# Performance work log

Measured on AMD Instinct MI355X. Metric: run time of the kernel, lower is better.

## Reference

```python
import jax, jax.numpy as jnp
import numpy as np

H, W, V = 32, 64, 13
B, C_IN = 8, 256
RADIUS = 6371.0 * 1000.0
NUM_LAT = H + 2
_j = np.arange(1, NUM_LAT - 1, dtype=np.float64)
_LATS = (90.0 - _j * 180.0 / (NUM_LAT - 1)) * np.pi / 180.0  # [32] radians
PIXEL_X = jnp.asarray(2.0 * np.pi * RADIUS * np.cos(_LATS) / W, dtype=jnp.float32).reshape(1, 1, H, 1)
PIXEL_Y = np.float32(np.pi * RADIUS / (H + 1))
_DZ = np.array([50, 50, 50, 50, 50, 75, 100, 100, 100, 125, 112, 75, 75], dtype=np.float32)
PIXEL_Z = jnp.asarray(_DZ).reshape(1, V, 1, 1)
PRESSURE = jnp.asarray([50, 100, 150, 200, 250, 300, 400, 500, 600, 700, 850, 925, 1000], dtype=jnp.float32).reshape(1, V, 1, 1)
M_Z = jnp.asarray(np.tril(np.ones((V, V), dtype=np.float32)) * _DZ[None, :])  # lower-tri integration matrix
LAT_GRID = jnp.asarray(_LATS, dtype=jnp.float32).reshape(1, 1, H, 1)

OMEGA, L_V, R_GAS, C_P, R_D = 7.29e-5, 2.5e6, 8.314, 1005.0, 287.0
DIFF_RATIO, DT, K_H, K_V = 0.05, 300.0, 15.0, 0.1
SIGMA, EMIS, PTHRESH = 5.67e-8, 0.7, 0.8
sg = jax.lax.stop_gradient


def d_x(f):  # periodic 4th-order diff along W, kernel [1,-8,0,8,-1]/12
    g = (jnp.roll(f, 2, 3) - 8.0 * jnp.roll(f, 1, 3) + 8.0 * jnp.roll(f, -1, 3) - jnp.roll(f, -2, 3)) / 12.0
    return g / PIXEL_X


def d_y(f):  # replicate-block padding along H, kernel [-1,8,0,-8,1]/12
    p = jnp.concatenate([f[:, :, :2], f, f[:, :, -2:]], axis=2)
    g = (-p[:, :, :-4] + 8.0 * p[:, :, 1:-3] - 8.0 * p[:, :, 3:-1] + p[:, :, 4:]) / 12.0
    return g / PIXEL_Y


def d_z(f):  # replicate-block padding along level dim (axis 1)
    p = jnp.concatenate([f[:, :2], f, f[:, -2:]], axis=1)
    g = (-p[:, :-4] + 8.0 * p[:, 1:-3] - 8.0 * p[:, 3:-1] + p[:, 4:]) / 12.0
    return g / PIXEL_Z


def integral_z(f):
    return jnp.einsum('ij,bjhw->bihw', M_Z, f)


def conv3x3(x, w, b):
    y = jax.lax.conv_general_dilated(x, w, (1, 1), ((1, 1), (1, 1)), dimension_numbers=('NCHW', 'OIHW', 'NCHW'))
    return y + b[None, :, None, None]


def batchnorm(x, g, b, eps=1e-5):  # training-mode BN (batch statistics)
    m = x.mean(axis=(0, 2, 3), keepdims=True)
    v = x.var(axis=(0, 2, 3), keepdims=True)
    return (x - m) / jnp.sqrt(v + eps) * g.reshape(1, -1, 1, 1) + b.reshape(1, -1, 1, 1)


def scale_tensor(t, a, b):
    mn, mx = sg(t.min()), sg(t.max())
    return (t - mn) / (mx - mn) * (b - a) + a


def scale_diff(d, x):
    mn, me, mx = sg(x.min()), sg(x.mean()), sg(x.max())
    return scale_tensor(d, (mn - me) * DIFF_RATIO, (mx - me) * DIFF_RATIO)


def avoid_inf(t, thr=1.0):
    t = jnp.where(jnp.abs(t) == 0.0, jnp.full_like(t, 0.1), t)
    return jnp.where(jnp.abs(t) < thr, jnp.sign(t) * thr, t)


def mixing(f):
    return K_H * (d_x(d_x(f)) + d_y(d_y(f))) + K_V * d_z(d_z(f))


def rad_cool(t):
    ta = t + 273.15
    return -(EMIS * SIGMA * ta ** 4) / (C_P * PRESSURE * 100.0 / (R_D * ta))


def saturation(t, z_z):
    rho = -1.0 / avoid_inf(z_z)
    p = rho * R_GAS * t
    tc = t - 273.15
    e_s = 6.112 * jnp.exp(scale_tensor(17.67 * tc / avoid_inf(tc + 243.5), -3.47, 3.01)) * 100.0
    return jnp.maximum(0.622 * e_s / avoid_inf(p - 0.378 * e_s), 1e-6)


def precip(q, q_s):
    rh = q / avoid_inf(q_s)
    rate = (rh > PTHRESH).astype(q.dtype) * (q - PTHRESH * q_s) / DT
    return rate, rate * L_V / C_P


def uv_dt(u, v, w, u_x, v_y, z_x, z_y):
    # u_x, v_y are held fixed across RK stages (stateful self.u_x/self.v_y in the original)
    f_cor = 2.0 * OMEGA * jnp.sin(LAT_GRID)
    u_t = -u * u_x - v * d_y(u) - w * d_z(u) + f_cor * v - z_x + mixing(u)
    v_t = -u * d_x(v) - v * v_y - w * d_z(v) - f_cor * u - z_y + mixing(v)
    return u_t, v_t


def t_dt(u, v, w, t, q, q_s, z_z):
    Q = -L_V * z_z * w
    _, lh = precip(q, q_s)
    return (Q - z_z * w) / C_P - u * d_x(t) - v * d_y(t) - w * d_z(t) + mixing(t) + rad_cool(t) + lh


def pde_forward(x, w_norm, b_norm, w_innorm, b_innorm, coef, gz, bz, gq, bq, gu, bu, gv, bv, gt, bt, gblk, bblk):
    h = conv3x3(x, w_norm, b_norm)  # [B, 65, H, W]
    z, q, u, v, t = jnp.split(h, 5, axis=1)
    z = batchnorm(z, gz, bz); q = batchnorm(q, gq, bq)
    u = batchnorm(u, gu, bu); v = batchnorm(v, gv, bv); t = batchnorm(t, gt, bt)
    z_x, z_y, z_z = d_x(z), d_y(z), d_z(z)
    u_x, v_y = d_x(u), d_y(v)
    w_vel = -integral_z(u_x + v_y)  # continuity: dw/dz = -(u_x + v_y)
    # --- RK4 momentum evolution ---
    k1u, k1v = uv_dt(u, v, w_vel, u_x, v_y, z_x, z_y)
    k2u, k2v = uv_dt(u + 0.5 * DT * k1u, v + 0.5 * DT * k1v, w_vel, u_x, v_y, z_x, z_y)
    k3u, k3v = uv_dt(u + 0.5 * DT * k2u, v + 0.5 * DT * k2v, w_vel, u_x, v_y, z_x, z_y)
    k4u, k4v = uv_dt(u + DT * k3u, v + DT * k3v, w_vel, u_x, v_y, z_x, z_y)
    u_new = u + sg(scale_diff((k1u + 2 * k2u + 2 * k3u + k4u) / 6.0 * DT, u))
    v_new = v + sg(scale_diff((k1v + 2 * k2v + 2 * k3v + k4v) / 6.0 * DT, v))
    # --- RK4 temperature evolution (q_s fixed from initial t) ---
    q_s = saturation(t, z_z)
    k1t = t_dt(u, v, w_vel, t, q, q_s, z_z)
    k2t = t_dt(u, v, w_vel, t + 0.5 * DT * k1t, q, q_s, z_z)
    k3t = t_dt(u, v, w_vel, t + 0.5 * DT * k2t, q, q_s, z_z)
    k4t = t_dt(u, v, w_vel, t + DT * k3t, q, q_s, z_z)
    t_new = t + sg(scale_diff((k1t + 2 * k2t + 2 * k3t + k4t) / 6.0 * DT, t))
    # geopotential tendency uses stateful self.t_t (last computed stage = k4t)
    z_t = integral_z(-R_GAS / PRESSURE * k4t)
    z_new = z + sg(scale_diff(z_t * DT, z))
    # moisture evolution
    pr, _ = precip(q, q_s)
    q_t = -u * d_x(q) - v * d_y(q) - w_vel * d_z(q) + mixing(q) - pr
    q_new = q + sg(scale_diff(q_t * DT, q))
    phys = jnp.concatenate([z_new, q_new, u_new, v_new, t_new], axis=1)
    out = coef * phys + (1.0 - coef) * h
    out = conv3x3(out, w_innorm, b_innorm)
    return batchnorm(out, gblk, bblk) + x


def setup_inputs() -> dict:
    key = jax.random.key(0)
    k0, k1, k2 = jax.random.split(key, 3)
    VD = V * 5
    ones13 = jnp.ones((V,), jnp.float32)
    zeros13 = jnp.zeros((V,), jnp.float32)
    return {
        'x': jax.random.normal(k0, (B, C_IN, H, W), jnp.float32),
        'w_norm': jax.random.normal(k1, (VD, C_IN, 3, 3), jnp.float32) * 0.02,
        'b_norm': jnp.zeros((VD,), jnp.float32),
        'w_innorm': jax.random.normal(k2, (C_IN, VD, 3, 3), jnp.float32) * 0.02,
        'b_innorm': jnp.zeros((C_IN,), jnp.float32),
        'coef': 0.5 * jnp.ones((1, VD, H, W), jnp.float32),
        'gz': 0.1 * ones13, 'bz': zeros13,
        'gq': 0.1 * ones13, 'bq': zeros13,
        'gu': 0.1 * ones13, 'bu': zeros13,
        'gv': 0.1 * ones13, 'bv': zeros13,
        'gt': 0.1 * ones13, 'bt': zeros13,
        'gblk': jnp.ones((C_IN,), jnp.float32),
        'bblk': jnp.zeros((C_IN,), jnp.float32),
    }


def reference(x, w_norm, b_norm, w_innorm, b_innorm, coef, gz, bz, gq, bq, gu, bu, gv, bv, gt, bt, gblk, bblk):
    return pde_forward(x, w_norm, b_norm, w_innorm, b_innorm, coef, gz, bz, gq, bq, gu, bu, gv, bv, gt, bt, gblk, bblk)
```

## Files before the change

### kernel.cpp

```cpp
#include <hip/hip_runtime.h>
#include <math.h>

#define DEVFN static __device__ __forceinline__

static constexpr int BB = 8, VV = 13, HH = 32, WW = 64;
static constexpr int NPLANE = HH * WW;
static constexpr int NF = BB * VV * NPLANE;
static constexpr int NHB = BB * 65 * NPLANE;

static constexpr float DT = 300.0f;
static constexpr float KHc = 15.0f, KVc = 0.1f;
static constexpr float OMEGAc = 7.29e-5f;
static constexpr float L_Vc = 2.5e6f;
static constexpr float R_GASc = 8.314f;
static constexpr float C_Pc = 1005.0f;
static constexpr float PTHc = 0.8f;
static constexpr float PYc  = (float)(3.14159265358979323846 * 6371000.0 / 33.0);
static constexpr float PXCc = (float)(2.0 * 3.14159265358979323846 * 6371000.0 / 64.0);
static constexpr double RCCd = 0.7 * 5.67e-8 * 287.0 / (1005.0 * 100.0);
static constexpr float FBIG = 3.402823466e38f;

__constant__ float cDZ[13]  = {50,50,50,50,50,75,100,100,100,125,112,75,75};
__constant__ float cZI[13] = {
  (float)(1.0/600.0), (float)(1.0/600.0), (float)(1.0/600.0), (float)(1.0/600.0), (float)(1.0/600.0),
  (float)(1.0/900.0), (float)(1.0/1200.0), (float)(1.0/1200.0), (float)(1.0/1200.0),
  (float)(1.0/1500.0), (float)(1.0/1344.0), (float)(1.0/900.0), (float)(1.0/900.0)};
__constant__ float cRC[13] = {
  (float)(-RCCd/50.0), (float)(-RCCd/100.0), (float)(-RCCd/150.0), (float)(-RCCd/200.0),
  (float)(-RCCd/250.0), (float)(-RCCd/300.0), (float)(-RCCd/400.0), (float)(-RCCd/500.0),
  (float)(-RCCd/600.0), (float)(-RCCd/700.0), (float)(-RCCd/850.0), (float)(-RCCd/925.0),
  (float)(-RCCd/1000.0)};
__constant__ float cZW[13] = {
  (float)(50.0*(-8.314/50.0)), (float)(50.0*(-8.314/100.0)), (float)(50.0*(-8.314/150.0)),
  (float)(50.0*(-8.314/200.0)), (float)(50.0*(-8.314/250.0)), (float)(75.0*(-8.314/300.0)),
  (float)(100.0*(-8.314/400.0)), (float)(100.0*(-8.314/500.0)), (float)(100.0*(-8.314/600.0)),
  (float)(125.0*(-8.314/700.0)), (float)(112.0*(-8.314/850.0)), (float)(75.0*(-8.314/925.0)),
  (float)(75.0*(-8.314/1000.0))};

typedef short bf16x8 __attribute__((ext_vector_type(8)));
typedef float f32x4 __attribute__((ext_vector_type(4)));

DEVFN int pmh(int r){ return r < 0 ? r + 2 : (r > HH - 1 ? r - 2 : r); }
DEVFN int pmv(int r){ return r < 0 ? r + 2 : (r > VV - 1 ? r - 2 : r); }
DEVFN float latOf(int h){ return (90.0f - (float)(h + 1) * (180.0f / 33.0f)) * 0.017453292519943295f; }
DEVFN float avoid_inf(float t){
  if (t == 0.0f) t = 0.1f;
  if (fabsf(t) < 1.0f) t = copysignf(1.0f, t);
  return t;
}
DEVFN unsigned short f2bf(float f){
  unsigned u = __float_as_uint(f);
  unsigned r = (u + 0x7fffu + ((u >> 16) & 1u)) >> 16;
  return (unsigned short)r;
}

DEVFN float d_xf(const float* __restrict__ F, int rb, int w, float invpx){
  return (F[rb + ((w + 62) & 63)] - 8.f * F[rb + ((w + 63) & 63)]
        + 8.f * F[rb + ((w + 1) & 63)] - F[rb + ((w + 2) & 63)]) * (1.f / 12.f) * invpx;
}
DEVFN float d_yf(const float* __restrict__ F, int bvbase, int h, int w){
  return (-F[bvbase + pmh(h - 2) * 64 + w] + 8.f * F[bvbase + pmh(h - 1) * 64 + w]
          - 8.f * F[bvbase + pmh(h + 1) * 64 + w] + F[bvbase + pmh(h + 2) * 64 + w]) * (1.f / 12.f) * (1.f / PYc);
}
DEVFN float d_zf(const float* __restrict__ F, int bbase, int v, int hw){
  return (-F[bbase + pmv(v - 2) * 2048 + hw] + 8.f * F[bbase + pmv(v - 1) * 2048 + hw]
          - 8.f * F[bbase + pmv(v + 1) * 2048 + hw] + F[bbase + pmv(v + 2) * 2048 + hw]) * cZI[v];
}
DEVFN float dxxf(const float* __restrict__ F, int rb, int w, float invpx){
  float s = F[rb + ((w + 60) & 63)] - 16.f * F[rb + ((w + 61) & 63)] + 64.f * F[rb + ((w + 62) & 63)]
          + 16.f * F[rb + ((w + 63) & 63)] - 130.f * F[rb + w] + 16.f * F[rb + ((w + 1) & 63)]
          + 64.f * F[rb + ((w + 2) & 63)] - 16.f * F[rb + ((w + 3) & 63)] + F[rb + ((w + 4) & 63)];
  return s * (1.f / 144.f) * invpx * invpx;
}
DEVFN float dyyf(const float* __restrict__ F, int bvbase, int h, int w){
  float g0 = d_yf(F, bvbase, pmh(h - 2), w);
  float g1 = d_yf(F, bvbase, pmh(h - 1), w);
  float g2 = d_yf(F, bvbase, pmh(h + 1), w);
  float g3 = d_yf(F, bvbase, pmh(h + 2), w);
  return (-g0 + 8.f * g1 - 8.f * g2 + g3) * (1.f / 12.f) * (1.f / PYc);
}
DEVFN float dzzf(const float* __restrict__ F, int bbase, int v, int hw){
  float g0 = d_zf(F, bbase, pmv(v - 2), hw);
  float g1 = d_zf(F, bbase, pmv(v - 1), hw);
  float g2 = d_zf(F, bbase, pmv(v + 1), hw);
  float g3 = d_zf(F, bbase, pmv(v + 2), hw);
  return (-g0 + 8.f * g1 - 8.f * g2 + g3) * cZI[v];
}

DEVFN float waveRedSum(float v){ for (int o = 32; o; o >>= 1) v += __shfl_down(v, o, 64); return v; }
DEVFN float waveRedMin(float v){ for (int o = 32; o; o >>= 1) v = fminf(v, __shfl_down(v, o, 64)); return v; }
DEVFN float waveRedMax(float v){ for (int o = 32; o; o >>= 1) v = fmaxf(v, __shfl_down(v, o, 64)); return v; }

template<int OP, int NWV>
static __device__ float blockRedN(float v){
  __shared__ float s[NWV];
  v = OP == 0 ? waveRedSum(v) : OP == 1 ? waveRedMin(v) : waveRedMax(v);
  int lane = threadIdx.x & 63, wid = threadIdx.x >> 6;
  __syncthreads();
  if (lane == 0) s[wid] = v;
  __syncthreads();
  float r = s[0];
  #pragma unroll
  for (int k = 1; k < NWV; ++k)
    r = OP == 0 ? r + s[k] : OP == 1 ? fminf(r, s[k]) : fmaxf(r, s[k]);
  return r;
}

struct GB { const float* g[5]; const float* b[5]; };

__global__ void __launch_bounds__(256) pre_k(const float* __restrict__ x,
    const float* __restrict__ w1, const float* __restrict__ w2,
    unsigned short* __restrict__ XT, unsigned short* __restrict__ wp1,
    unsigned short* __restrict__ wp2)
{
  int blk = blockIdx.x, t = threadIdx.x;
  if (blk < 1024){
    __shared__ float tile[16 * 68];
    int zz = blk >> 8, rem = blk & 255;
    int b = rem >> 5, h = rem & 31;
    for (int p = zz * 4; p < zz * 4 + 4; ++p){
      int cbase = p * 16;
      __syncthreads();
      {
        int cl = t >> 4, w4 = (t & 15) * 4;
        float4 v = *(const float4*)(x + (((size_t)(b * 256 + cbase + cl) * 32 + h) * 64 + w4));
        tile[cl * 68 + w4 + 0] = v.x; tile[cl * 68 + w4 + 1] = v.y;
        tile[cl * 68 + w4 + 2] = v.z; tile[cl * 68 + w4 + 3] = v.w;
      }
      __syncthreads();
      {
        int w = t >> 2, c4 = (t & 3) * 4;
        ushort4 o;
        o.x = f2bf(tile[(c4 + 0) * 68 + w]);
        o.y = f2bf(tile[(c4 + 1) * 68 + w]);
        o.z = f2bf(tile[(c4 + 2) * 68 + w]);
        o.w = f2bf(tile[(c4 + 3) * 68 + w]);
        *(ushort4*)(XT + (((size_t)(b * 32 + h) * 64 + w) * 256 + cbase + c4)) = o;
      }
    }
  } else {
    const int T1 = 9 * 80 * 256;
    const int T2 = 9 * 256 * 96;
    int idx = (blk - 1024) * 256 + t;
    if (idx < T1){
      int dir = idx / (80 * 256);
      int r = idx - dir * (80 * 256);
      int co = r / 256, ci = r - co * 256;
      float v = (co < 65) ? w1[((size_t)(co * 256 + ci)) * 9 + dir] : 0.f;
      wp1[idx] = f2bf(v);
    } else if (idx < T1 + T2){
      int j = idx - T1;
      int dir = j / (256 * 96);
      int r = j - dir * (256 * 96);
      int co = r / 96, ci = r - co * 96;
      float v = (ci < 65) ? w2[((size_t)(co * 65 + ci)) * 9 + dir] : 0.f;
      wp2[j] = f2bf(v);
    }
  }
}

template<int CIT, int CIL, int CO, int COp, int NW, int MF, int SWZ>
__global__ void __launch_bounds__(NW * 64) conv_mfma_k(
    const unsigned short* __restrict__ XT, const unsigned short* __restrict__ Wp,
    const float* __restrict__ bias, float* __restrict__ out, float* __restrict__ bnp)
{
  __shared__ __align__(16) unsigned short Xl[3 * 34 * CIL];
  const int C8 = CIL / 8;
  int tid = threadIdx.x;
  int bx = blockIdx.x, b = blockIdx.y;
  int h = bx >> 1, p0 = (bx & 1) << 5;
  int bh = b * 64 + bx;
  int wid = tid >> 6, lane = tid & 63;
  int l15 = lane & 15, q = lane >> 4;

  f32x4 acc[MF][2];
  #pragma unroll
  for (int mf = 0; mf < MF; ++mf)
    #pragma unroll
    for (int nf = 0; nf < 2; ++nf){ f32x4 z = {0.f, 0.f, 0.f, 0.f}; acc[mf][nf] = z; }

  for (int cp = 0; cp < CIT / CIL; ++cp){
    if (cp) __syncthreads();
    for (int idx = tid; idx < 3 * 34 * C8; idx += NW * 64){
      int r = idx / (34 * C8);
      int rest = idx - r * (34 * C8);
      int j = rest / C8;
      int c8 = rest - j * C8;
      int hh = h + r - 1;
      int gw = p0 - 1 + j;
      uint4 val = make_uint4(0, 0, 0, 0);
      if (hh >= 0 && hh < 32 && gw >= 0 && gw < 64)
        val = *(const uint4*)(XT + (((size_t)(b * 32 + hh) * 64 + gw) * CIT + cp * CIL + c8 * 8));
      int dst = (r * 34 + j) * CIL + ((c8 * 8) ^ ((j & SWZ) << 3));
      *(uint4*)(Xl + dst) = val;
    }
    __syncthreads();

    for (int dir = 0; dir < 9; ++dir){
      int dy = dir / 3, dx = dir - dy * 3;
      #pragma unroll
      for (int kc = 0; kc < CIL / 32; ++kc){
        int kb = kc * 32 + q * 8;
        bf16x8 a[MF];
        #pragma unroll
        for (int mf = 0; mf < MF; ++mf){
          int co = wid * (MF * 16) + mf * 16 + l15;
          a[mf] = *(const bf16x8*)(Wp + ((size_t)(dir * COp + co) * CIT + cp * CIL + kb));
        }
        #pragma unroll
        for (int nf = 0; nf < 2; ++nf){
          int j = nf * 16 + l15 + dx;
          bf16x8 bfrag = *(const bf16x8*)(Xl + ((dy * 34 + j) * CIL + (kb ^ ((j & SWZ) << 3))));
          #pragma unroll
          for (int mf = 0; mf < MF; ++mf)
            acc[mf][nf] = __builtin_amdgcn_mfma_f32_16x16x32_bf16(a[mf], bfrag, acc[mf][nf], 0, 0, 0);
        }
      }
    }
  }
  #pragma unroll
  for (int mf = 0; mf < MF; ++mf){
    #pragma unroll
    for (int r = 0; r < 4; ++r){
      int co = wid * (MF * 16) + mf * 16 + q * 4 + r;
      if (CO != COp && co >= CO) continue;
      float bv = bias[co];
      float sv = 0.f, sq = 0.f;
      #pragma unroll
      for (int nf = 0; nf < 2; ++nf){
        int pix = nf * 16 + l15;
        float val = acc[mf][nf][r] + bv;
        out[(size_t)(b * CO + co) * 2048 + h * 64 + p0 + pix] = val;
        sv += val; sq += val * val;
      }
      #pragma unroll
      for (int off = 8; off; off >>= 1){
        sv += __shfl_xor(sv, off, 16);
        sq += __shfl_xor(sq, off, 16);
      }
      if (l15 == 0){
        bnp[((size_t)co * 512 + bh) * 2]     = sv;
        bnp[((size_t)co * 512 + bh) * 2 + 1] = sq;
      }
    }
  }
}

__global__ void __launch_bounds__(256) prep_k(const float* __restrict__ hb,
  const float* __restrict__ bnp1, GB gb,
  float* __restrict__ Fz, float* __restrict__ Fq, float* __restrict__ Fu,
  float* __restrict__ Fvf, float* __restrict__ Ft,
  float* __restrict__ zx, float* __restrict__ zy, float* __restrict__ zz,
  float* __restrict__ ux, float* __restrict__ vy, float* __restrict__ wv,
  float* __restrict__ partS)
{
  __shared__ float As[65], Bs[65];
  int blk = blockIdx.x, t = threadIdx.x;
  {
    int wvid = t >> 6, lane = t & 63;
    for (int ch = wvid; ch < 65; ch += 4){
      const float4* pp = (const float4*)(bnp1 + (size_t)ch * 1024) + lane * 4;
      float s = 0.f, sq = 0.f;
      #pragma unroll
      for (int k = 0; k < 4; ++k){ float4 v = pp[k]; s += v.x + v.z; sq += v.y + v.w; }
      s = waveRedSum(s); sq = waveRedSum(sq);
      if (!lane){
        float m = s * (1.f / 16384.f);
        float var = sq * (1.f / 16384.f) - m * m;
        float rstd = rsqrtf(var + 1e-5f);
        int f = ch / 13, k = ch - f * 13;
        float g = gb.g[f][k], bbv = gb.b[f][k];
        As[ch] = g * rstd; Bs[ch] = bbv - m * g * rstd;
      }
    }
  }
  __syncthreads();

  int part = blk >> 6;
  int col = ((blk & 63) << 8) | t;
  int b = col >> 11, p = col & 2047, h = p >> 6, w = p & 63;
  int hbase = b * 65 * NPLANE;
  auto hn = [&](int ch, int hh, int ww)->float {
    return hb[hbase + ch * 2048 + hh * 64 + ww] * As[ch] + Bs[ch];
  };
  int fb = (b * 13) * 2048 + p;
  float lat = latOf(h);
  float invpx = 1.0f / (PXCc * cosf(lat));
  int wm2 = (w + 62) & 63, wm1 = (w + 63) & 63, wpl1 = (w + 1) & 63, wpl2 = (w + 2) & 63;
  int hm2 = pmh(h - 2), hm1 = pmh(h - 1), hp1 = pmh(h + 1), hp2 = pmh(h + 2);
  float fmn = FBIG, fmx = -FBIG, fsm = 0.f, smn = FBIG, smx = -FBIG;
  if (part < 5){
    int ch0 = part * 13;
    float c[13];
    #pragma unroll
    for (int v = 0; v < 13; ++v) c[v] = hn(ch0 + v, h, w);
    float* Fdst = part == 0 ? Fz : part == 1 ? Fq : part == 2 ? Fu : part == 3 ? Fvf : Ft;
    #pragma unroll
    for (int v = 0; v < 13; ++v) Fdst[fb + v * 2048] = c[v];
    if (part == 0){
      #pragma unroll
      for (int v = 0; v < 13; ++v){
        zz[fb + v * 2048] = (-c[pmv(v - 2)] + 8.f * c[pmv(v - 1)] - 8.f * c[pmv(v + 1)] + c[pmv(v + 2)]) * cZI[v];
        float zxv = (hn(v, h, wm2) - 8.f * hn(v, h, wm1) + 8.f * hn(v, h, wpl1) - hn(v, h, wpl2)) * (1.f / 12.f) * invpx;
        float zyv = (-hn(v, hm2, w) + 8.f * hn(v, hm1, w) - 8.f * hn(v, hp1, w) + hn(v, hp2, w)) * (1.f / 12.f) * (1.f / PYc);
        zx[fb + v * 2048] = zxv; zy[fb + v * 2048] = zyv;
      }
    }
    if (part == 2){
      #pragma unroll
      for (int v = 0; v < 13; ++v){
        float uxv = (hn(26 + v, h, wm2) - 8.f * hn(26 + v, h, wm1) + 8.f * hn(26 + v, h, wpl1) - hn(26 + v, h, wpl2)) * (1.f / 12.f) * invpx;
        ux[fb + v * 2048] = uxv;
      }
    }
    if (part == 3){
      #pragma unroll
      for (int v = 0; v < 13; ++v){
        float vyv = (-hn(39 + v, hm2, w) + 8.f * hn(39 + v, hm1, w) - 8.f * hn(39 + v, hp1, w) + hn(39 + v, hp2, w)) * (1.f / 12.f) * (1.f / PYc);
        vy[fb + v * 2048] = vyv;
      }
    }
    if (part == 4){
      #pragma unroll
      for (int v = 0; v < 13; ++v){
        float tcc = c[v] - 273.15f;
        float arg = 17.67f * tcc / avoid_inf(tcc + 243.5f);
        smn = fminf(smn, arg); smx = fmaxf(smx, arg);
      }
    }
    #pragma unroll
    for (int v = 0; v < 13; ++v){ fmn = fminf(fmn, c[v]); fmx = fmaxf(fmx, c[v]); fsm += c[v]; }
  } else {
    float cum = 0.f;
    #pragma unroll
    for (int v = 0; v < 13; ++v){
      float uxv = (hn(26 + v, h, wm2) - 8.f * hn(26 + v, h, wm1) + 8.f * hn(26 + v, h, wpl1) - hn(26 + v, h, wpl2)) * (1.f / 12.f) * invpx;
      float vyv = (-hn(39 + v, hm2, w) + 8.f * hn(39 + v, hm1, w) - 8.f * hn(39 + v, hp1, w) + hn(39 + v, hp2, w)) * (1.f / 12.f) * (1.f / PYc);
      cum += cDZ[v] * (uxv + vyv);
      wv[fb + v * 2048] = -cum;
    }
  }
  float* pb = partS + blk * 17;
  float r;
  r = blockRedN<1,4>(smn); if (!t) pb[0] = r;
  r = blockRedN<2,4>(smx); if (!t) pb[1] = r;
  #pragma unroll
  for (int f = 0; f < 5; ++f){
    r = blockRedN<1,4>(part == f ? fmn : FBIG);  if (!t) pb[2 + f * 3] = r;
    r = blockRedN<2,4>(part == f ? fmx : -FBIG); if (!t) pb[3 + f * 3] = r;
    r = blockRedN<0,4>(part == f ? fsm : 0.f);   if (!t) pb[4 + f * 3] = r;
  }
}

template<int STAGE>
__global__ void __launch_bounds__(256) stage_k(
  const float* __restrict__ U, const float* __restrict__ Vf, const float* __restrict__ T,
  const float* __restrict__ Fu, const float* __restrict__ Fvf, const float* __restrict__ Ft,
  const float* __restrict__ Fq,
  const float* __restrict__ ux, const float* __restrict__ vy,
  const float* __restrict__ zx, const float* __restrict__ zy,
  const float* __restrict__ wv, const float* __restrict__ zz,
  const float* __restrict__ partS,
  float* C0, float* prr,
  float* Uo, float* Vo, float* To,
  float* duA, float* dvA, float* dtA, float* k4t, float* qtA,
  float* pduv, float* pdt, float* pqt, float cnext)
{
  int part = blockIdx.y;
  int blk = blockIdx.x, t = threadIdx.x;
  int i = blk * 256 + t;
  int w = i & 63, h = (i >> 6) & 31;
  int bv = i >> 11;
  int v = bv % 13;
  int bvbase = bv * 2048;
  int rb = bvbase + h * 64;
  int bbase = (bv - v) * 2048;
  int hw = h * 64 + w;
  float lat = latOf(h);
  float invpx = 1.0f / (PXCc * cosf(lat));
  float wvi = wv[i];

  if (part == 0){
    float Ui = U[i], Vi = Vf[i];
    float fcor = 2.0f * OMEGAc * sinf(lat);
    float dyU = d_yf(U, bvbase, h, w);
    float dzU = d_zf(U, bbase, v, hw);
    float mixU = KHc * (dxxf(U, rb, w, invpx) + dyyf(U, bvbase, h, w)) + KVc * dzzf(U, bbase, v, hw);
    float ku = -Ui * ux[i] - Vi * dyU - wvi * dzU + fcor * Vi - zx[i] + mixU;
    if (STAGE == 1) duA[i] = ku;
    else if (STAGE < 4) duA[i] += 2.f * ku;
    else {
      float au = duA[i] + ku; duA[i] = au;
      float m0 = blockRedN<1,4>(au), m1 = blockRedN<2,4>(au);
      if (!t){ pduv[blk * 4] = m0; pduv[blk * 4 + 1] = m1; }
    }
    if (STAGE < 4) Uo[i] = Fu[i] + cnext * ku;
  } else if (part == 1){
    float Ui = U[i], Vi = Vf[i];
    float fcor = 2.0f * OMEGAc * sinf(lat);
    float dxV = d_xf(Vf, rb, w, invpx);
    float dzV = d_zf(Vf, bbase, v, hw);
    float mixV = KHc * (dxxf(Vf, rb, w, invpx) + dyyf(Vf, bvbase, h, w)) + KVc * dzzf(Vf, bbase, v, hw);
    float kv = -Ui * dxV - Vi * vy[i] - wvi * dzV - fcor * Ui - zy[i] + mixV;
    if (STAGE == 1) dvA[i] = kv;
    else if (STAGE < 4) dvA[i] += 2.f * kv;
    else {
      float av = dvA[i] + kv; dvA[i] = av;
      float m2 = blockRedN<1,4>(av), m3 = blockRedN<2,4>(av);
      if (!t){ pduv[blk * 4 + 2] = m2; pduv[blk * 4 + 3] = m3; }
    }
    if (STAGE < 4) Vo[i] = Fvf[i] + cnext * kv;
  } else if (part == 2){
    float ss = 0.f, off = 0.f;
    if (STAGE == 1){
      float v0 = partS[t * 17], v1 = partS[t * 17 + 1];
      if (t < 128){
        v0 = fminf(v0, partS[(t + 256) * 17]);
        v1 = fmaxf(v1, partS[(t + 256) * 17 + 1]);
      }
      float smn = blockRedN<1,4>(v0);
      float smx = blockRedN<2,4>(v1);
      ss = (3.01f + 3.47f) / (smx - smn);
      off = -3.47f - smn * ss;
    }
    float Ti = T[i];
    float Fui = Fu[i], Fvi = Fvf[i];
    float C0i;
    if (STAGE == 1){
      float zzi = zz[i], qi = Fq[i];
      float rho = -1.0f / avoid_inf(zzi);
      float p = rho * R_GASc * Ti;
      float tcc = Ti - 273.15f;
      float arg = 17.67f * tcc / avoid_inf(tcc + 243.5f);
      float es = 6.112f * expf(arg * ss + off) * 100.0f;
      float qs = fmaxf(0.622f * es / avoid_inf(p - 0.378f * es), 1e-6f);
      float rh = qi / avoid_inf(qs);
      float rate = (rh > PTHc) ? (qi - PTHc * qs) * (1.0f / DT) : 0.0f;
      prr[i] = rate;
      C0i = -(L_Vc + 1.0f) * zzi * wvi * (1.0f / C_Pc) + rate * (L_Vc / C_Pc);
      C0[i] = C0i;
    } else {
      C0i = C0[i];
    }
    float dxT = d_xf(T, rb, w, invpx);
    float dyT = d_yf(T, bvbase, h, w);
    float dzT = d_zf(T, bbase, v, hw);
    float mixT = KHc * (dxxf(T, rb, w, invpx) + dyyf(T, bvbase, h, w)) + KVc * dzzf(T, bbase, v, hw);
    float ta = Ti + 273.15f;
    float t2 = ta * ta;
    float ta5 = t2 * t2 * ta;
    float rc = cRC[v] * ta5;
    float kt = C0i - Fui * dxT - Fvi * dyT - wvi * dzT + mixT + rc;
    if (STAGE == 1) dtA[i] = kt;
    else if (STAGE < 4) dtA[i] += 2.f * kt;
    else {
      float at = dtA[i] + kt; dtA[i] = at; k4t[i] = kt;
      float m4 = blockRedN<1,4>(at), m5 = blockRedN<2,4>(at);
      if (!t){ pdt[blk * 2] = m4; pdt[blk * 2 + 1] = m5; }
    }
    if (STAGE < 4) To[i] = Ft[i] + cnext * kt;
  } else if (STAGE == 2){
    float Fui = Fu[i], Fvi = Fvf[i];
    float qtv = -Fui * d_xf(Fq, rb, w, invpx) - Fvi * d_yf(Fq, bvbase, h, w) - wvi * d_zf(Fq, bbase, v, hw)
              + KHc * (dxxf(Fq, rb, w, invpx) + dyyf(Fq, bvbase, h, w)) + KVc * dzzf(Fq, bbase, v, hw) - prr[i];
    qtA[i] = qtv;
    float m0 = blockRedN<1,4>(qtv), m1 = blockRedN<2,4>(qtv);
    if (!t){ pqt[blk * 2] = m0; pqt[blk * 2 + 1] = m1; }
  }
}

__global__ void __launch_bounds__(64) zt_k(const float* __restrict__ k4t, float* __restrict__ zt, float* __restrict__ pmm)
{
  int col = blockIdx.x * 64 + threadIdx.x;
  int b = col >> 11, p = col & 2047;
  int fb = b * 13 * 2048 + p;
  float cum = 0.f, mn = FBIG, mx = -FBIG;
  #pragma unroll
  for (int v = 0; v < 13; ++v){
    cum += cZW[v] * k4t[fb + v * 2048];
    zt[fb + v * 2048] = cum;
    mn = fminf(mn, cum); mx = fmaxf(mx, cum);
  }
  mn = waveRedMin(mn); mx = waveRedMax(mx);
  if (!threadIdx.x){ pmm[blockIdx.x * 2] = mn; pmm[blockIdx.x * 2 + 1] = mx; }
}

__global__ void __launch_bounds__(256) outmid_fused_k(
  const float* __restrict__ hb,
  const float* __restrict__ Fz, const float* __restrict__ Fq, const float* __restrict__ Fu,
  const float* __restrict__ Fvf, const float* __restrict__ Ft,
  const float* __restrict__ ztA, const float* __restrict__ qtA,
  const float* __restrict__ duA, const float* __restrict__ dvA, const float* __restrict__ dtA,
  const float* __restrict__ coef, const float* __restrict__ partS,
  const float* __restrict__ pduv, const float* __restrict__ pdt,
  const float* __restrict__ pqt, const float* __restrict__ pzt,
  unsigned short* __restrict__ MT)
{
  __shared__ float tileBig[65 * 66];
  int blk = blockIdx.x, t = threadIdx.x;

  float fmn[5] = {FBIG, FBIG, FBIG, FBIG, FBIG};
  float fmx[5] = {-FBIG, -FBIG, -FBIG, -FBIG, -FBIG};
  float fsm[5] = {0.f, 0.f, 0.f, 0.f, 0.f};
  #pragma unroll 1
  for (int r0 = t; r0 < 384; r0 += 256){
    const float* pr = partS + r0 * 17;
    #pragma unroll
    for (int f = 0; f < 5; ++f){
      fmn[f] = fminf(fmn[f], pr[2 + f * 3]);
      fmx[f] = fmaxf(fmx[f], pr[3 + f * 3]);
      fsm[f] += pr[4 + f * 3];
    }
  }
  #pragma unroll
  for (int f = 0; f < 5; ++f){
    fmn[f] = blockRedN<1,4>(fmn[f]);
    fmx[f] = blockRedN<2,4>(fmx[f]);
    fsm[f] = blockRedN<0,4>(fsm[f]);
  }
  float dumn = FBIG, dumx = -FBIG, dvmn = FBIG, dvmx = -FBIG, dtmn = FBIG, dtmx = -FBIG;
  float qmn = FBIG, qmx = -FBIG;
  #pragma unroll 1
  for (int r0 = t; r0 < 832; r0 += 256){
    dumn = fminf(dumn, pduv[r0 * 4]);     dumx = fmaxf(dumx, pduv[r0 * 4 + 1]);
    dvmn = fminf(dvmn, pduv[r0 * 4 + 2]); dvmx = fmaxf(dvmx, pduv[r0 * 4 + 3]);
    dtmn = fminf(dtmn, pdt[r0 * 2]);      dtmx = fmaxf(dtmx, pdt[r0 * 2 + 1]);
    qmn = fminf(qmn, pqt[r0 * 2]);        qmx = fmaxf(qmx, pqt[r0 * 2 + 1]);
  }
  float zmn = pzt[t * 2], zmx = pzt[t * 2 + 1];
  dumn = blockRedN<1,4>(dumn); dumx = blockRedN<2,4>(dumx);
  dvmn = blockRedN<1,4>(dvmn); dvmx = blockRedN<2,4>(dvmx);
  dtmn = blockRedN<1,4>(dtmn); dtmx = blockRedN<2,4>(dtmx);
  qmn = blockRedN<1,4>(qmn);   qmx = blockRedN<2,4>(qmx);
  zmn = blockRedN<1,4>(zmn);   zmx = blockRedN<2,4>(zmx);

  float scf[5], off2[5];
  {
    float rmn[5] = {zmn, qmn, dumn, dvmn, dtmn};
    float rmx[5] = {zmx, qmx, dumx, dvmx, dtmx};
    float cfs[5] = {DT, DT, DT / 6.f, DT / 6.f, DT / 6.f};
    #pragma unroll
    for (int f = 0; f < 5; ++f){
      float mnf = fmn[f], mef = fsm[f] * (1.0f / (float)NF), mxf = fmx[f];
      float aa = (mnf - mef) * 0.05f, b2 = (mxf - mef) * 0.05f;
      float cf = cfs[f];
      float dmn = rmn[f] * cf, dmx = rmx[f] * cf;
      float s = (b2 - aa) / (dmx - dmn);
      scf[f] = s * cf; off2[f] = aa - dmn * s;
    }
  }

  int b = blk >> 5, h = blk & 31;
  #pragma unroll 1
  for (int idx = t; idx < 65 * 64; idx += 256){
    int c = idx >> 6, w = idx & 63;
    int f = c / 13, v = c - f * 13;
    int fi = (b * 13 + v) * 2048 + h * 64 + w;
    const float *Fp, *Rp;
    switch (f){
      case 0: Fp = Fz;  Rp = ztA; break;
      case 1: Fp = Fq;  Rp = qtA; break;
      case 2: Fp = Fu;  Rp = duA; break;
      case 3: Fp = Fvf; Rp = dvA; break;
      default: Fp = Ft; Rp = dtA; break;
    }
    float phys = Fp[fi] + Rp[fi] * scf[f] + off2[f];
    float cf = coef[c * 2048 + h * 64 + w];
    float hbv = hb[((size_t)(b * 65 + c)) * 2048 + h * 64 + w];
    tileBig[c * 66 + w] = cf * phys + (1.0f - cf) * hbv;
  }
  __syncthreads();
  #pragma unroll 1
  for (int ph = 0; ph < 6; ++ph){
    int cbase = ph * 16;
    int w = t >> 2, c4 = (t & 3) * 4;
    int c0 = cbase + c4;
    ushort4 o;
    o.x = (c0 + 0 < 65) ? f2bf(tileBig[(c0 + 0) * 66 + w]) : (unsigned short)0;
    o.y = (c0 + 1 < 65) ? f2bf(tileBig[(c0 + 1) * 66 + w]) : (unsigned short)0;
    o.z = (c0 + 2 < 65) ? f2bf(tileBig[(c0 + 2) * 66 + w]) : (unsigned short)0;
    o.w = (c0 + 3 < 65) ? f2bf(tileBig[(c0 + 3) * 66 + w]) : (unsigned short)0;
    *(ushort4*)(MT + (((size_t)(b * 32 + h) * 64 + w) * 96 + c0)) = o;
  }
}

__global__ void __launch_bounds__(256) final_k(float* __restrict__ y, const float* __restrict__ x,
  const float* __restrict__ bnp2, const float* __restrict__ gblk, const float* __restrict__ bblk)
{
  int blk = blockIdx.x, t = threadIdx.x;
  int c = (blk >> 1) & 255;
  float4 pv = ((const float4*)(bnp2 + (size_t)c * 1024))[t];
  float s = pv.x + pv.z, sq = pv.y + pv.w;
  s = blockRedN<0,4>(s); sq = blockRedN<0,4>(sq);
  float m = s * (1.0f / 16384.0f);
  float var = sq * (1.0f / 16384.0f) - m * m;
  float rstd = rsqrtf(var + 1e-5f);
  float a = gblk[c] * rstd, bb = bblk[c] - m * gblk[c] * rstd;
  int e4 = blk * 256 + t;
  float4 v = ((const float4*)y)[e4];
  float4 xv = ((const float4*)x)[e4];
  v.x = v.x * a + bb + xv.x;
  v.y = v.y * a + bb + xv.y;
  v.z = v.z * a + bb + xv.z;
  v.w = v.w * a + bb + xv.w;
  ((float4*)y)[e4] = v;
}

extern "C" void kernel_launch(void* const* d_in, const int* in_sizes, int n_in,
                              void* d_out, int out_size, void* d_ws, size_t ws_size,
                              hipStream_t stream)
{
  (void)in_sizes; (void)n_in; (void)out_size; (void)ws_size;
  const float* x        = (const float*)d_in[0];
  const float* w_norm   = (const float*)d_in[1];
  const float* b_norm   = (const float*)d_in[2];
  const float* w_innorm = (const float*)d_in[3];
  const float* b_innorm = (const float*)d_in[4];
  const float* coef     = (const float*)d_in[5];
  GB gb;
  for (int f = 0; f < 5; ++f){
    gb.g[f] = (const float*)d_in[6 + 2 * f];
    gb.b[f] = (const float*)d_in[7 + 2 * f];
  }
  const float* gblk = (const float*)d_in[16];
  const float* bblk = (const float*)d_in[17];
  float* yout = (float*)d_out;

  float* ws = (float*)d_ws;
  size_t off = 0;
  auto alloc = [&](size_t n){ float* p = ws + off; off += n; return p; };
  float* hb  = alloc(NHB);
  float* Fz  = alloc(NF); float* Fq  = alloc(NF); float* Fu  = alloc(NF);
  float* Fvf = alloc(NF); float* Ft  = alloc(NF);
  float* zx  = alloc(NF); float* zy  = alloc(NF); float* zz  = alloc(NF);
  float* ux  = alloc(NF); float* vy  = alloc(NF); float* wvel = alloc(NF);
  float* C0  = alloc(NF); float* prr = alloc(NF);
  float* Ua  = alloc(NF); float* Ub  = alloc(NF); float* Va  = alloc(NF); float* Vb = alloc(NF);
  float* Ta  = alloc(NF); float* Tb  = alloc(NF);
  float* duA = alloc(NF); float* dvA = alloc(NF); float* dtA = alloc(NF);
  float* k4t = alloc(NF); float* ztA = alloc(NF); float* qtA = alloc(NF);
  float* part1 = alloc(384 * 17 + 4);
  float* pduv = alloc(832 * 4); float* pdt = alloc(832 * 2);
  float* pqt  = alloc(832 * 2); float* pzt = alloc(256 * 2);
  float* bnp1 = alloc(65 * 512 * 2);
  float* bnp2 = alloc(256 * 512 * 2);
  float* Wp1f = alloc(9 * 80 * 256 / 2);
  float* Wp2f = alloc(9 * 256 * 96 / 2);
  unsigned short* Wp1 = (unsigned short*)Wp1f;
  unsigned short* Wp2 = (unsigned short*)Wp2f;
  unsigned short* XT = (unsigned short*)Ua;
  unsigned short* MT = (unsigned short*)C0;

  pre_k<<<2608, 256, 0, stream>>>(x, w_norm, w_innorm, XT, Wp1, Wp2);
  conv_mfma_k<256, 128, 65, 80, 5, 1, 7><<<dim3(64, 8), 5 * 64, 0, stream>>>(XT, Wp1, b_norm, hb, bnp1);
  prep_k<<<384, 256, 0, stream>>>(hb, bnp1, gb, Fz, Fq, Fu, Fvf, Ft, zx, zy, zz, ux, vy, wvel, part1);
  stage_k<1><<<dim3(NF / 256, 3), 256, 0, stream>>>(Fu, Fvf, Ft, Fu, Fvf, Ft, Fq, ux, vy, zx, zy, wvel, zz, part1,
      C0, prr, Ua, Va, Ta, duA, dvA, dtA, k4t, qtA, pduv, pdt, pqt, 0.5f * DT);
  stage_k<2><<<dim3(NF / 256, 4), 256, 0, stream>>>(Ua, Va, Ta, Fu, Fvf, Ft, Fq, ux, vy, zx, zy, wvel, zz, part1,
      C0, prr, Ub, Vb, Tb, duA, dvA, dtA, k4t, qtA, pduv, pdt, pqt, 0.5f * DT);
  stage_k<3><<<dim3(NF / 256, 3), 256, 0, stream>>>(Ub, Vb, Tb, Fu, Fvf, Ft, Fq, ux, vy, zx, zy, wvel, zz, part1,
      C0, prr, Ua, Va, Ta, duA, dvA, dtA, k4t, qtA, pduv, pdt, pqt, DT);
  stage_k<4><<<dim3(NF / 256, 3), 256, 0, stream>>>(Ua, Va, Ta, Fu, Fvf, Ft, Fq, ux, vy, zx, zy, wvel, zz, part1,
      C0, prr, Ub, Vb, Tb, duA, dvA, dtA, k4t, qtA, pduv, pdt, pqt, 0.f);
  zt_k<<<256, 64, 0, stream>>>(k4t, ztA, pzt);
  outmid_fused_k<<<256, 256, 0, stream>>>(hb, Fz, Fq, Fu, Fvf, Ft, ztA, qtA, duA, dvA, dtA,
      coef, part1, pduv, pdt, pqt, pzt, MT);
  conv_mfma_k<96, 96, 256, 256, 8, 2, 3><<<dim3(64, 8), 8 * 64, 0, stream>>>(MT, Wp2, b_innorm, yout, bnp2);
  final_k<<<4096, 256, 0, stream>>>(yout, x, bnp2, gblk, bblk);
}
```

Baseline: 189.4 us.

## Merge RK stage parts into one (b,h)-row block, fuse vertical z-integral

Each RK stage kernel now launches one 832-thread block per (batch, latitude row) that covers all 13 levels and 64 longitudes. A single thread computes the U, V and T tendencies, where before a separate grid slice handled each, so shared loads of U, V and wv are reused. Stage 4 also does the cumulative vertical integral of the temperature tendency in shared memory, which removes the separate zt_k kernel and the k4t buffer. The per-block partial min/max arrays shrink to 256 entries, so the later reduction no longer loops, and pre_k uses more, smaller transpose blocks. The price is large blocks with heavier register pressure, which may lower occupancy, plus wide 13-wave block reductions.

```diff
diff --git a/kernel.cpp b/kernel.cpp
--- a/kernel.cpp
+++ b/kernel.cpp
@@ -114,11 +114,11 @@
     unsigned short* __restrict__ wp2)
 {
   int blk = blockIdx.x, t = threadIdx.x;
-  if (blk < 1024){
+  if (blk < 2048){
     __shared__ float tile[16 * 68];
     int zz = blk >> 8, rem = blk & 255;
     int b = rem >> 5, h = rem & 31;
-    for (int p = zz * 4; p < zz * 4 + 4; ++p){
+    for (int p = zz * 2; p < zz * 2 + 2; ++p){
       int cbase = p * 16;
       __syncthreads();
       {
@@ -141,7 +141,7 @@
   } else {
     const int T1 = 9 * 80 * 256;
     const int T2 = 9 * 256 * 96;
-    int idx = (blk - 1024) * 256 + t;
+    int idx = (blk - 2048) * 256 + t;
     if (idx < T1){
       int dir = idx / (80 * 256);
       int r = idx - dir * (80 * 256);
@@ -353,7 +353,7 @@
 }
 
 template<int STAGE>
-__global__ void __launch_bounds__(256) stage_k(
+__global__ void __launch_bounds__(832) stage_k(
   const float* __restrict__ U, const float* __restrict__ Vf, const float* __restrict__ T,
   const float* __restrict__ Fu, const float* __restrict__ Fvf, const float* __restrict__ Ft,
   const float* __restrict__ Fq,
@@ -363,126 +363,115 @@
   const float* __restrict__ partS,
   float* C0, float* prr,
   float* Uo, float* Vo, float* To,
-  float* duA, float* dvA, float* dtA, float* k4t, float* qtA,
-  float* pduv, float* pdt, float* pqt, float cnext)
+  float* duA, float* dvA, float* dtA, float* qtA, float* ztA,
+  float* pduv, float* pdt, float* pqt, float* pzt, float cnext)
 {
-  int part = blockIdx.y;
+  __shared__ float Zk[13 * 64];
   int blk = blockIdx.x, t = threadIdx.x;
-  int i = blk * 256 + t;
-  int w = i & 63, h = (i >> 6) & 31;
-  int bv = i >> 11;
-  int v = bv % 13;
+
+  float ss = 0.f, off = 0.f;
+  if (STAGE == 1){
+    float v0 = (t < 384) ? partS[t * 17] : FBIG;
+    float v1 = (t < 384) ? partS[t * 17 + 1] : -FBIG;
+    float smn = blockRedN<1,13>(v0);
+    float smx = blockRedN<2,13>(v1);
+    ss = (3.01f + 3.47f) / (smx - smn);
+    off = -3.47f - smn * ss;
+  }
+
+  int b = blk >> 5, h = blk & 31;
+  int v = t >> 6, w = t & 63;
+  int bv = b * 13 + v;
   int bvbase = bv * 2048;
   int rb = bvbase + h * 64;
-  int bbase = (bv - v) * 2048;
+  int bbase = (b * 13) * 2048;
   int hw = h * 64 + w;
+  int i = bvbase + hw;
   float lat = latOf(h);
   float invpx = 1.0f / (PXCc * cosf(lat));
+  float fcor = 2.0f * OMEGAc * sinf(lat);
   float wvi = wv[i];
-
-  if (part == 0){
-    float Ui = U[i], Vi = Vf[i];
-    float fcor = 2.0f * OMEGAc * sinf(lat);
-    float dyU = d_yf(U, bvbase, h, w);
-    float dzU = d_zf(U, bbase, v, hw);
-    float mixU = KHc * (dxxf(U, rb, w, invpx) + dyyf(U, bvbase, h, w)) + KVc * dzzf(U, bbase, v, hw);
-    float ku = -Ui * ux[i] - Vi * dyU - wvi * dzU + fcor * Vi - zx[i] + mixU;
-    if (STAGE == 1) duA[i] = ku;
-    else if (STAGE < 4) duA[i] += 2.f * ku;
-    else {
-      float au = duA[i] + ku; duA[i] = au;
-      float m0 = blockRedN<1,4>(au), m1 = blockRedN<2,4>(au);
-      if (!t){ pduv[blk * 4] = m0; pduv[blk * 4 + 1] = m1; }
-    }
-    if (STAGE < 4) Uo[i] = Fu[i] + cnext * ku;
-  } else if (part == 1){
-    float Ui = U[i], Vi = Vf[i];
-    float fcor = 2.0f * OMEGAc * sinf(lat);
-    float dxV = d_xf(Vf, rb, w, invpx);
-    float dzV = d_zf(Vf, bbase, v, hw);
-    float mixV = KHc * (dxxf(Vf, rb, w, invpx) + dyyf(Vf, bvbase, h, w)) + KVc * dzzf(Vf, bbase, v, hw);
-    float kv = -Ui * dxV - Vi * vy[i] - wvi * dzV - fcor * Ui - zy[i] + mixV;
-    if (STAGE == 1) dvA[i] = kv;
-    else if (STAGE < 4) dvA[i] += 2.f * kv;
-    else {
-      float av = dvA[i] + kv; dvA[i] = av;
-      float m2 = blockRedN<1,4>(av), m3 = blockRedN<2,4>(av);
-      if (!t){ pduv[blk * 4 + 2] = m2; pduv[blk * 4 + 3] = m3; }
-    }
-    if (STAGE < 4) Vo[i] = Fvf[i] + cnext * kv;
-  } else if (part == 2){
-    float ss = 0.f, off = 0.f;
-    if (STAGE == 1){
-      float v0 = partS[t * 17], v1 = partS[t * 17 + 1];
-      if (t < 128){
-        v0 = fminf(v0, partS[(t + 256) * 17]);
-        v1 = fmaxf(v1, partS[(t + 256) * 17 + 1]);
-      }
-      float smn = blockRedN<1,4>(v0);
-      float smx = blockRedN<2,4>(v1);
-      ss = (3.01f + 3.47f) / (smx - smn);
-      off = -3.47f - smn * ss;
-    }
-    float Ti = T[i];
-    float Fui = Fu[i], Fvi = Fvf[i];
-    float C0i;
-    if (STAGE == 1){
-      float zzi = zz[i], qi = Fq[i];
-      float rho = -1.0f / avoid_inf(zzi);
-      float p = rho * R_GASc * Ti;
-      float tcc = Ti - 273.15f;
-      float arg = 17.67f * tcc / avoid_inf(tcc + 243.5f);
-      float es = 6.112f * expf(arg * ss + off) * 100.0f;
-      float qs = fmaxf(0.622f * es / avoid_inf(p - 0.378f * es), 1e-6f);
-      float rh = qi / avoid_inf(qs);
-      float rate = (rh > PTHc) ? (qi - PTHc * qs) * (1.0f / DT) : 0.0f;
-      prr[i] = rate;
-      C0i = -(L_Vc + 1.0f) * zzi * wvi * (1.0f / C_Pc) + rate * (L_Vc / C_Pc);
-      C0[i] = C0i;
-    } else {
-      C0i = C0[i];
-    }
-    float dxT = d_xf(T, rb, w, invpx);
-    float dyT = d_yf(T, bvbase, h, w);
-    float dzT = d_zf(T, bbase, v, hw);
-    float mixT = KHc * (dxxf(T, rb, w, invpx) + dyyf(T, bvbase, h, w)) + KVc * dzzf(T, bbase, v, hw);
-    float ta = Ti + 273.15f;
-    float t2 = ta * ta;
-    float ta5 = t2 * t2 * ta;
-    float rc = cRC[v] * ta5;
-    float kt = C0i - Fui * dxT - Fvi * dyT - wvi * dzT + mixT + rc;
-    if (STAGE == 1) dtA[i] = kt;
-    else if (STAGE < 4) dtA[i] += 2.f * kt;
-    else {
-      float at = dtA[i] + kt; dtA[i] = at; k4t[i] = kt;
-      float m4 = blockRedN<1,4>(at), m5 = blockRedN<2,4>(at);
-      if (!t){ pdt[blk * 2] = m4; pdt[blk * 2 + 1] = m5; }
-    }
-    if (STAGE < 4) To[i] = Ft[i] + cnext * kt;
-  } else if (STAGE == 2){
-    float Fui = Fu[i], Fvi = Fvf[i];
+  float Ui = U[i], Vi = Vf[i], Ti = T[i];
+  float Fui = (STAGE == 1) ? Ui : Fu[i];
+  float Fvi = (STAGE == 1) ? Vi : Fvf[i];
+
+  float dyU = d_yf(U, bvbase, h, w);
+  float dzU = d_zf(U, bbase, v, hw);
+  float dxV = d_xf(Vf, rb, w, invpx);
+  float dzV = d_zf(Vf, bbase, v, hw);
+  float mixU = KHc * (dxxf(U, rb, w, invpx) + dyyf(U, bvbase, h, w)) + KVc * dzzf(U, bbase, v, hw);
+  float mixV = KHc * (dxxf(Vf, rb, w, invpx) + dyyf(Vf, bvbase, h, w)) + KVc * dzzf(Vf, bbase, v, hw);
+  float ku = -Ui * ux[i] - Vi * dyU - wvi * dzU + fcor * Vi - zx[i] + mixU;
+  float kv = -Ui * dxV - Vi * vy[i] - wvi * dzV - fcor * Ui - zy[i] + mixV;
+
+  float C0i;
+  if (STAGE == 1){
+    float zzi = zz[i], qi = Fq[i];
+    float rho = -1.0f / avoid_inf(zzi);
+    float p = rho * R_GASc * Ti;
+    float tcc = Ti - 273.15f;
+    float arg = 17.67f * tcc / avoid_inf(tcc + 243.5f);
+    float es = 6.112f * expf(arg * ss + off) * 100.0f;
+    float qs = fmaxf(0.622f * es / avoid_inf(p - 0.378f * es), 1e-6f);
+    float rh = qi / avoid_inf(qs);
+    float rate = (rh > PTHc) ? (qi - PTHc * qs) * (1.0f / DT) : 0.0f;
+    prr[i] = rate;
+    C0i = -(L_Vc + 1.0f) * zzi * wvi * (1.0f / C_Pc) + rate * (L_Vc / C_Pc);
+    C0[i] = C0i;
+  } else {
+    C0i = C0[i];
+  }
+
+  float dxT = d_xf(T, rb, w, invpx);
+  float dyT = d_yf(T, bvbase, h, w);
+  float dzT = d_zf(T, bbase, v, hw);
+  float mixT = KHc * (dxxf(T, rb, w, invpx) + dyyf(T, bvbase, h, w)) + KVc * dzzf(T, bbase, v, hw);
+  float ta = Ti + 273.15f;
+  float t2 = ta * ta;
+  float ta5 = t2 * t2 * ta;
+  float rc = cRC[v] * ta5;
+  float kt = C0i - Fui * dxT - Fvi * dyT - wvi * dzT + mixT + rc;
+
+  if (STAGE == 1){ duA[i] = ku; dvA[i] = kv; dtA[i] = kt; }
+  else if (STAGE < 4){ duA[i] += 2.f * ku; dvA[i] += 2.f * kv; dtA[i] += 2.f * kt; }
+  else {
+    float au = duA[i] + ku, av = dvA[i] + kv, at = dtA[i] + kt;
+    duA[i] = au; dvA[i] = av; dtA[i] = at;
+    Zk[v * 64 + w] = cZW[v] * kt;
+    float m0 = blockRedN<1,13>(au), m1 = blockRedN<2,13>(au);
+    float m2 = blockRedN<1,13>(av), m3 = blockRedN<2,13>(av);
+    float m4 = blockRedN<1,13>(at), m5 = blockRedN<2,13>(at);
+    if (!t){
+      float* pp = pduv + blk * 4;
+      pp[0] = m0; pp[1] = m1; pp[2] = m2; pp[3] = m3;
+      pdt[blk * 2] = m4; pdt[blk * 2 + 1] = m5;
+    }
+    if (t < 64){
+      float cum = 0.f, mn = FBIG, mx = -FBIG;
+      #pragma unroll
+      for (int j = 0; j < 13; ++j){
+        cum += Zk[j * 64 + t];
+        ztA[bbase + j * 2048 + h * 64 + t] = cum;
+        mn = fminf(mn, cum); mx = fmaxf(mx, cum);
+      }
+      mn = waveRedMin(mn); mx = waveRedMax(mx);
+      if (!t){ pzt[blk * 2] = mn; pzt[blk * 2 + 1] = mx; }
+    }
+  }
+  if (STAGE < 4){
+    float Fti = (STAGE == 1) ? Ti : Ft[i];
+    Uo[i] = Fui + cnext * ku;
+    Vo[i] = Fvi + cnext * kv;
+    To[i] = Fti + cnext * kt;
+  }
+
+  if (STAGE == 2){
     float qtv = -Fui * d_xf(Fq, rb, w, invpx) - Fvi * d_yf(Fq, bvbase, h, w) - wvi * d_zf(Fq, bbase, v, hw)
               + KHc * (dxxf(Fq, rb, w, invpx) + dyyf(Fq, bvbase, h, w)) + KVc * dzzf(Fq, bbase, v, hw) - prr[i];
     qtA[i] = qtv;
-    float m0 = blockRedN<1,4>(qtv), m1 = blockRedN<2,4>(qtv);
+    float m0 = blockRedN<1,13>(qtv), m1 = blockRedN<2,13>(qtv);
     if (!t){ pqt[blk * 2] = m0; pqt[blk * 2 + 1] = m1; }
   }
-}
-
-__global__ void __launch_bounds__(64) zt_k(const float* __restrict__ k4t, float* __restrict__ zt, float* __restrict__ pmm)
-{
-  int col = blockIdx.x * 64 + threadIdx.x;
-  int b = col >> 11, p = col & 2047;
-  int fb = b * 13 * 2048 + p;
-  float cum = 0.f, mn = FBIG, mx = -FBIG;
-  #pragma unroll
-  for (int v = 0; v < 13; ++v){
-    cum += cZW[v] * k4t[fb + v * 2048];
-    zt[fb + v * 2048] = cum;
-    mn = fminf(mn, cum); mx = fmaxf(mx, cum);
-  }
-  mn = waveRedMin(mn); mx = waveRedMax(mx);
-  if (!threadIdx.x){ pmm[blockIdx.x * 2] = mn; pmm[blockIdx.x * 2 + 1] = mx; }
 }
 
 __global__ void __launch_bounds__(256) outmid_fused_k(
@@ -518,16 +507,11 @@
     fmx[f] = blockRedN<2,4>(fmx[f]);
     fsm[f] = blockRedN<0,4>(fsm[f]);
   }
-  float dumn = FBIG, dumx = -FBIG, dvmn = FBIG, dvmx = -FBIG, dtmn = FBIG, dtmx = -FBIG;
-  float qmn = FBIG, qmx = -FBIG;
-  #pragma unroll 1
-  for (int r0 = t; r0 < 832; r0 += 256){
-    dumn = fminf(dumn, pduv[r0 * 4]);     dumx = fmaxf(dumx, pduv[r0 * 4 + 1]);
-    dvmn = fminf(dvmn, pduv[r0 * 4 + 2]); dvmx = fmaxf(dvmx, pduv[r0 * 4 + 3]);
-    dtmn = fminf(dtmn, pdt[r0 * 2]);      dtmx = fmaxf(dtmx, pdt[r0 * 2 + 1]);
-    qmn = fminf(qmn, pqt[r0 * 2]);        qmx = fmaxf(qmx, pqt[r0 * 2 + 1]);
-  }
-  float zmn = pzt[t * 2], zmx = pzt[t * 2 + 1];
+  float dumn = pduv[t * 4],     dumx = pduv[t * 4 + 1];
+  float dvmn = pduv[t * 4 + 2], dvmx = pduv[t * 4 + 3];
+  float dtmn = pdt[t * 2],      dtmx = pdt[t * 2 + 1];
+  float qmn = pqt[t * 2],       qmx = pqt[t * 2 + 1];
+  float zmn = pzt[t * 2],       zmx = pzt[t * 2 + 1];
   dumn = blockRedN<1,4>(dumn); dumx = blockRedN<2,4>(dumx);
   dvmn = blockRedN<1,4>(dvmn); dvmx = blockRedN<2,4>(dvmx);
   dtmn = blockRedN<1,4>(dtmn); dtmx = blockRedN<2,4>(dtmx);
@@ -638,10 +622,10 @@
   float* Ua  = alloc(NF); float* Ub  = alloc(NF); float* Va  = alloc(NF); float* Vb = alloc(NF);
   float* Ta  = alloc(NF); float* Tb  = alloc(NF);
   float* duA = alloc(NF); float* dvA = alloc(NF); float* dtA = alloc(NF);
-  float* k4t = alloc(NF); float* ztA = alloc(NF); float* qtA = alloc(NF);
+  float* ztA = alloc(NF); float* qtA = alloc(NF);
   float* part1 = alloc(384 * 17 + 4);
-  float* pduv = alloc(832 * 4); float* pdt = alloc(832 * 2);
-  float* pqt  = alloc(832 * 2); float* pzt = alloc(256 * 2);
+  float* pduv = alloc(256 * 4); float* pdt = alloc(256 * 2);
+  float* pqt  = alloc(256 * 2); float* pzt = alloc(256 * 2);
   float* bnp1 = alloc(65 * 512 * 2);
   float* bnp2 = alloc(256 * 512 * 2);
   float* Wp1f = alloc(9 * 80 * 256 / 2);
@@ -651,18 +635,17 @@
   unsigned short* XT = (unsigned short*)Ua;
   unsigned short* MT = (unsigned short*)C0;
 
-  pre_k<<<2608, 256, 0, stream>>>(x, w_norm, w_innorm, XT, Wp1, Wp2);
+  pre_k<<<3632, 256, 0, stream>>>(x, w_norm, w_innorm, XT, Wp1, Wp2);
   conv_mfma_k<256, 128, 65, 80, 5, 1, 7><<<dim3(64, 8), 5 * 64, 0, stream>>>(XT, Wp1, b_norm, hb, bnp1);
   prep_k<<<384, 256, 0, stream>>>(hb, bnp1, gb, Fz, Fq, Fu, Fvf, Ft, zx, zy, zz, ux, vy, wvel, part1);
-  stage_k<1><<<dim3(NF / 256, 3), 256, 0, stream>>>(Fu, Fvf, Ft, Fu, Fvf, Ft, Fq, ux, vy, zx, zy, wvel, zz, part1,
-      C0, prr, Ua, Va, Ta, duA, dvA, dtA, k4t, qtA, pduv, pdt, pqt, 0.5f * DT);
-  stage_k<2><<<dim3(NF / 256, 4), 256, 0, stream>>>(Ua, Va, Ta, Fu, Fvf, Ft, Fq, ux, vy, zx, zy, wvel, zz, part1,
-      C0, prr, Ub, Vb, Tb, duA, dvA, dtA, k4t, qtA, pduv, pdt, pqt, 0.5f * DT);
-  stage_k<3><<<dim3(NF / 256, 3), 256, 0, stream>>>(Ub, Vb, Tb, Fu, Fvf, Ft, Fq, ux, vy, zx, zy, wvel, zz, part1,
-      C0, prr, Ua, Va, Ta, duA, dvA, dtA, k4t, qtA, pduv, pdt, pqt, DT);
-  stage_k<4><<<dim3(NF / 256, 3), 256, 0, stream>>>(Ua, Va, Ta, Fu, Fvf, Ft, Fq, ux, vy, zx, zy, wvel, zz, part1,
-      C0, prr, Ub, Vb, Tb, duA, dvA, dtA, k4t, qtA, pduv, pdt, pqt, 0.f);
-  zt_k<<<256, 64, 0, stream>>>(k4t, ztA, pzt);
+  stage_k<1><<<256, 832, 0, stream>>>(Fu, Fvf, Ft, Fu, Fvf, Ft, Fq, ux, vy, zx, zy, wvel, zz, part1,
+      C0, prr, Ua, Va, Ta, duA, dvA, dtA, qtA, ztA, pduv, pdt, pqt, pzt, 0.5f * DT);
+  stage_k<2><<<256, 832, 0, stream>>>(Ua, Va, Ta, Fu, Fvf, Ft, Fq, ux, vy, zx, zy, wvel, zz, part1,
+      C0, prr, Ub, Vb, Tb, duA, dvA, dtA, qtA, ztA, pduv, pdt, pqt, pzt, 0.5f * DT);
+  stage_k<3><<<256, 832, 0, stream>>>(Ub, Vb, Tb, Fu, Fvf, Ft, Fq, ux, vy, zx, zy, wvel, zz, part1,
+      C0, prr, Ua, Va, Ta, duA, dvA, dtA, qtA, ztA, pduv, pdt, pqt, pzt, DT);
+  stage_k<4><<<256, 832, 0, stream>>>(Ua, Va, Ta, Fu, Fvf, Ft, Fq, ux, vy, zx, zy, wvel, zz, part1,
+      C0, prr, Ub, Vb, Tb, duA, dvA, dtA, qtA, ztA, pduv, pdt, pqt, pzt, 0.f);
   outmid_fused_k<<<256, 256, 0, stream>>>(hb, Fz, Fq, Fu, Fvf, Ft, ztA, qtA, duA, dvA, dtA,
       coef, part1, pduv, pdt, pqt, pzt, MT);
   conv_mfma_k<96, 96, 256, 256, 8, 2, 3><<<dim3(64, 8), 8 * 64, 0, stream>>>(MT, Wp2, b_innorm, yout, bnp2);
```

Measured after the change: 206.4 us. +9.0%, slower.
